# Kernel tuning notes

Measured on AMD Instinct MI355X. Metric: run time of the kernel, lower is better.

The kernel has to match this reference:

```python
import jax, jax.numpy as jnp
import numpy as np
from functools import partial

H = 1024  # lstm_num_hidden
OUT_LEN = 96


def _cell(x, h, c, Wih, Whh, b):
    # PyTorch LSTM cell, gate order (i, f, g, o). x:[B,D] h,c:[B,H]
    g = x @ Wih.T + h @ Whh.T + b
    i, f, gg, o = jnp.split(g, 4, axis=-1)
    i = jax.nn.sigmoid(i)
    f = jax.nn.sigmoid(f)
    o = jax.nn.sigmoid(o)
    c = f * c + i * jnp.tanh(gg)
    h = o * jnp.tanh(c)
    return h, c


def _lstm_layer(xs, Wih, Whh, b):
    # xs: [B, T, D] -> (ys [B,T,H], h_T [B,H], c_T [B,H])
    B = xs.shape[0]
    pre = jnp.einsum('btd,gd->btg', xs, Wih) + b  # precompute input projection

    def step(carry, p):
        h, c = carry
        g = p + h @ Whh.T
        i, f, gg, o = jnp.split(g, 4, axis=-1)
        i = jax.nn.sigmoid(i)
        f = jax.nn.sigmoid(f)
        o = jax.nn.sigmoid(o)
        c = f * c + i * jnp.tanh(gg)
        h = o * jnp.tanh(c)
        return (h, c), h

    h0 = jnp.zeros((B, H), xs.dtype)
    c0 = jnp.zeros((B, H), xs.dtype)
    (h, c), ys = jax.lax.scan(step, (h0, c0), jnp.swapaxes(pre, 0, 1))
    return jnp.swapaxes(ys, 0, 1), h, c


def setup_inputs() -> dict:
    key = jax.random.key(0)
    ks = jax.random.split(key, 16)
    s = 1.0 / np.sqrt(H)  # torch LSTM/Linear init scale
    u = lambda k, shape: jax.random.uniform(k, shape, jnp.float32, -s, s)
    inp = {
        'x': jax.random.normal(ks[0], (256, 336, 1), jnp.float32),
        'enc_Wih0': u(ks[1], (4 * H, 1)),
        'enc_Whh0': u(ks[2], (4 * H, H)),
        'enc_b0': u(ks[3], (4 * H,)),
        'enc_Wih1': u(ks[4], (4 * H, H)),
        'enc_Whh1': u(ks[5], (4 * H, H)),
        'enc_b1': u(ks[6], (4 * H,)),
        'dec_Wih0': u(ks[7], (4 * H, 1)),
        'dec_Whh0': u(ks[8], (4 * H, H)),
        'dec_b0': u(ks[9], (4 * H,)),
        'dec_Wih1': u(ks[10], (4 * H, H)),
        'dec_Whh1': u(ks[11], (4 * H, H)),
        'dec_b1': u(ks[12], (4 * H,)),
        'fc_W': u(ks[13], (1, H)),
        'fc_b': u(ks[14], (1,)),
    }
    return inp


def reference(x, enc_Wih0, enc_Whh0, enc_b0, enc_Wih1, enc_Whh1, enc_b1,
              dec_Wih0, dec_Whh0, dec_b0, dec_Wih1, dec_Whh1, dec_b1,
              fc_W, fc_b):
    # ----- encoder: 2-layer LSTM over x, keep only final (h, c) per layer -----
    ys0, h0, c0 = _lstm_layer(x, enc_Wih0, enc_Whh0, enc_b0)
    _, h1, c1 = _lstm_layer(ys0, enc_Wih1, enc_Whh1, enc_b1)

    xt = x[:, -1, -1:]  # [B, 1] last value of last feature

    def dec_step(carry, _):
        h0, c0, h1, c1, xt = carry
        h0, c0 = _cell(xt, h0, c0, dec_Wih0, dec_Whh0, dec_b0)
        h1, c1 = _cell(h0, h1, c1, dec_Wih1, dec_Whh1, dec_b1)
        y = h1 @ fc_W.T + fc_b  # [B, 1]
        return (h0, c0, h1, c1, y), y

    _, ys = jax.lax.scan(dec_step, (h0, c0, h1, c1, xt), None, length=OUT_LEN)
    return jnp.swapaxes(ys, 0, 1)  # [B, OUT_LEN, 1]
```

## Files before the change

### kernel.cpp

```cpp
#include <hip/hip_runtime.h>

typedef short short8 __attribute__((ext_vector_type(8)));
typedef float f32x4 __attribute__((ext_vector_type(4)));

#define SMEM_BYTES (65536 + 1024)

__device__ __forceinline__ unsigned short f2bf(float x) {
    unsigned int u = __float_as_uint(x);
    u += 0x7FFFu + ((u >> 16) & 1u);
    return (unsigned short)(u >> 16);
}

__device__ __forceinline__ float sigmoidf_(float x) {
    return 1.0f / (1.0f + __expf(-x));
}

__device__ __forceinline__ float tanhf_(float x) {
    float ax = fabsf(x);
    float e = __expf(2.0f * ax);
    float t = 1.0f - 2.0f / (e + 1.0f);
    return copysignf(t, x);
}

__device__ __forceinline__ void gl_lds16(const void* g, void* l) {
    __builtin_amdgcn_global_load_lds(
        (const __attribute__((address_space(1))) void*)g,
        (__attribute__((address_space(3))) void*)l, 16, 0, 0);
}


template<int K>
__device__ __forceinline__ void lstm_tile(
    int idx,
    const unsigned short* __restrict__ A1,
    const unsigned short* __restrict__ A2,
    const unsigned short* __restrict__ W,
    const float* __restrict__ bias,
    const float* __restrict__ xvec, int xstride,
    const float* __restrict__ Wx,
    float* __restrict__ c,
    unsigned short* __restrict__ hout,
    const float* __restrict__ fcW,
    const float* __restrict__ fcb,
    float* __restrict__ yout)
{
    extern __shared__ char smem_raw[];
    float* T0  = (float*)smem_raw;
    float* T1  = (float*)(smem_raw + 17408);
    float* red = (float*)(smem_raw + 65536);

    constexpr int KS = K / 4;
    constexpr int NC = KS / 32;
    constexpr int KC = K / 32;
    const int tid  = threadIdx.x;
    const int lane = tid & 63;
    const int wave = tid >> 6;
    const int g  = idx >> 6;
    const int ug = idx & 63;
    const int mb = g * 64;
    const int ub = ug * 16;

    const unsigned short* Af = (K == 1024) ? A1 : (wave < 2 ? A1 : A2);
    const int kcA0 = (wave * NC) & 31;
    const int kcW0 = wave * NC;
    const unsigned short* ap = Af + ((size_t)(g * 4) * 32 + kcA0) * 512 + lane * 8;
    const unsigned short* bp = W + ((size_t)(ug * KC + kcW0) * 4) * 512 + lane * 8;

    char* stg = smem_raw + wave * 16384;

    f32x4 acc[4][4];
#pragma unroll
    for (int i = 0; i < 4; ++i)
#pragma unroll
        for (int j = 0; j < 4; ++j) acc[i][j] = (f32x4){0.f, 0.f, 0.f, 0.f};

    auto STAGE = [&](int cc, int buf) {
        char* dst = stg + buf * 8192;
        const unsigned short* asrc = ap + cc * 512;
        const unsigned short* bsrc = bp + cc * 2048;
#pragma unroll
        for (int mi = 0; mi < 4; ++mi)
            gl_lds16(asrc + mi * 16384, dst + mi * 1024);
#pragma unroll
        for (int gt = 0; gt < 4; ++gt)
            gl_lds16(bsrc + gt * 512, dst + 4096 + gt * 1024);
    };
    auto CONSUME = [&](int buf) {
        const char* src = stg + buf * 8192;
        short8 a[4], b[4];
#pragma unroll
        for (int p = 0; p < 4; ++p)
            a[p] = *(const short8*)(src + p * 1024 + lane * 16);
#pragma unroll
        for (int p = 0; p < 4; ++p)
            b[p] = *(const short8*)(src + 4096 + p * 1024 + lane * 16);
#pragma unroll
        for (int mi = 0; mi < 4; ++mi)
#pragma unroll
            for (int gt = 0; gt < 4; ++gt)
                acc[mi][gt] = __builtin_amdgcn_mfma_f32_16x16x32_bf16(
                    a[mi], b[gt], acc[mi][gt], 0, 0, 0);
    };

    STAGE(0, 0);
#pragma unroll
    for (int cc = 0; cc < NC; ++cc) {
        STAGE(cc + 1, (cc + 1) & 1);
        asm volatile("s_waitcnt vmcnt(8)" ::: "memory");
        __builtin_amdgcn_sched_barrier(0);
        CONSUME(cc & 1);
    }
    asm volatile("s_waitcnt vmcnt(0)" ::: "memory");
    __syncthreads();

    const int q = lane >> 4;
    const int m = lane & 15;
    float* Tw = (wave & 1) ? T1 : T0;
    if (wave < 2) {
#pragma unroll
        for (int mi = 0; mi < 4; ++mi)
#pragma unroll
            for (int gt = 0; gt < 4; ++gt)
#pragma unroll
                for (int r = 0; r < 4; ++r)
                    Tw[(mi * 16 + q * 4 + r) * 68 + gt * 16 + m] = acc[mi][gt][r];
    }
    __syncthreads();
    if (wave >= 2) {
#pragma unroll
        for (int mi = 0; mi < 4; ++mi)
#pragma unroll
            for (int gt = 0; gt < 4; ++gt)
#pragma unroll
                for (int r = 0; r < 4; ++r)
                    Tw[(mi * 16 + q * 4 + r) * 68 + gt * 16 + m] += acc[mi][gt][r];
    }
    __syncthreads();

    const int lrow = tid >> 2;
    const int uq   = tid & 3;
    const int br   = mb + lrow;
    const int u0   = ub + uq * 4;
    const int toff = lrow * 68 + uq * 4;

    auto gate4 = [&](int gofs) -> float4 {
        float4 a = *(const float4*)(T0 + toff + gofs);
        float4 b = *(const float4*)(T1 + toff + gofs);
        return make_float4(a.x + b.x, a.y + b.y, a.z + b.z, a.w + b.w);
    };
    float4 GI = gate4(0), GF = gate4(16), GG = gate4(32), GO = gate4(48);
    float4 bI = *(const float4*)(bias + u0);
    float4 bF = *(const float4*)(bias + 1024 + u0);
    float4 bG = *(const float4*)(bias + 2048 + u0);
    float4 bO = *(const float4*)(bias + 3072 + u0);
    float4 wI = {0,0,0,0}, wF = {0,0,0,0}, wG = {0,0,0,0}, wO = {0,0,0,0};
    float xv = 0.f;
    if (xvec) {
        xv = xvec[br * xstride];
        wI = *(const float4*)(Wx + u0);
        wF = *(const float4*)(Wx + 1024 + u0);
        wG = *(const float4*)(Wx + 2048 + u0);
        wO = *(const float4*)(Wx + 3072 + u0);
    }
    float4 cc = *(const float4*)(c + (size_t)br * 1024 + u0);

    auto cellc = [&](float gi, float gf, float gg, float go, float cold, float& hO) -> float {
        float i = sigmoidf_(gi);
        float f = sigmoidf_(gf);
        float o = sigmoidf_(go);
        float cn = f * cold + i * tanhf_(gg);
        hO = o * tanhf_(cn);
        return cn;
    };
    float h0v, h1v, h2v, h3v;
    float4 cn;
    cn.x = cellc(GI.x + bI.x + xv * wI.x, GF.x + bF.x + xv * wF.x,
                 GG.x + bG.x + xv * wG.x, GO.x + bO.x + xv * wO.x, cc.x, h0v);
    cn.y = cellc(GI.y + bI.y + xv * wI.y, GF.y + bF.y + xv * wF.y,
                 GG.y + bG.y + xv * wG.y, GO.y + bO.y + xv * wO.y, cc.y, h1v);
    cn.z = cellc(GI.z + bI.z + xv * wI.z, GF.z + bF.z + xv * wF.z,
                 GG.z + bG.z + xv * wG.z, GO.z + bO.z + xv * wO.z, cc.z, h2v);
    cn.w = cellc(GI.w + bI.w + xv * wI.w, GF.w + bF.w + xv * wF.w,
                 GG.w + bG.w + xv * wG.w, GO.w + bO.w + xv * wO.w, cc.w, h3v);
    *(float4*)(c + (size_t)br * 1024 + u0) = cn;

    {
        const int rg = br >> 4, ml = br & 15;
        const int kc = u0 >> 5, qq = (u0 >> 3) & 3, jo = u0 & 7;
        ushort4 hu;
        hu.x = f2bf(h0v); hu.y = f2bf(h1v); hu.z = f2bf(h2v); hu.w = f2bf(h3v);
        *(ushort4*)(hout + ((size_t)(rg * 32 + kc) * 64 + qq * 16 + ml) * 8 + jo) = hu;
    }

    if (fcW) {
        float4 fw = *(const float4*)(fcW + u0);
        float fcp = h0v * fw.x + h1v * fw.y + h2v * fw.z + h3v * fw.w;
        red[uq * 64 + lrow] = fcp;
        __syncthreads();
        if (tid < 64) {
            float s = red[tid] + red[64 + tid] + red[128 + tid] + red[192 + tid];
            if (ub == 0) s += fcb[0];
            atomicAdd(yout + (size_t)(mb + tid) * 96, s);
        }
    }
}

__global__ __launch_bounds__(256)
__attribute__((amdgpu_waves_per_eu(2, 2)))
void k_enc_step(
    int t,
    const float* __restrict__ x,
    const float* __restrict__ Wih0, const float* __restrict__ b0,
    const unsigned short* __restrict__ Wenc0,
    const unsigned short* __restrict__ Wenc1, const float* __restrict__ b1,
    unsigned short* h0a, unsigned short* h0b,
    unsigned short* h1a, unsigned short* h1b,
    float* c0, float* c1)
{
    unsigned short* h0[2] = {h0a, h0b};
    unsigned short* h1[2] = {h1a, h1b};
    const int blk = blockIdx.x;
    if (blk < 256) {
        if (t >= 336) return;
        lstm_tile<1024>(blk, h0[(t + 1) & 1], nullptr, Wenc0, b0,
                        x + t, 336, Wih0, c0, h0[t & 1],
                        nullptr, nullptr, nullptr);
    } else {
        const int u = t - 1;
        if (u < 0) return;
        lstm_tile<2048>(blk - 256, h0[u & 1], h1[(u + 1) & 1], Wenc1, b1,
                        nullptr, 0, nullptr, c1, h1[u & 1],
                        nullptr, nullptr, nullptr);
    }
}

__global__ __launch_bounds__(256)
__attribute__((amdgpu_waves_per_eu(2, 2)))
void k_dec0(
    int s,
    const float* __restrict__ x,
    const float* __restrict__ dout,
    const float* __restrict__ Wih0, const float* __restrict__ b0,
    const unsigned short* __restrict__ Wdec0,
    unsigned short* h0a, unsigned short* h0b, float* c0)
{
    unsigned short* h0[2] = {h0a, h0b};
    const float* xv; int xs;
    if (s == 0) { xv = x + 335; xs = 336; }
    else        { xv = dout + (s - 1); xs = 96; }
    lstm_tile<1024>(blockIdx.x, h0[(s + 1) & 1], nullptr, Wdec0, b0,
                    xv, xs, Wih0, c0, h0[s & 1],
                    nullptr, nullptr, nullptr);
}

__global__ __launch_bounds__(256)
__attribute__((amdgpu_waves_per_eu(2, 2)))
void k_dec1(
    int s,
    const unsigned short* __restrict__ Wdec1, const float* __restrict__ b1,
    unsigned short* h0a, unsigned short* h0b,
    unsigned short* h1a, unsigned short* h1b,
    float* c1,
    const float* __restrict__ fcW, const float* __restrict__ fcb,
    float* __restrict__ dout)
{
    unsigned short* h0[2] = {h0a, h0b};
    unsigned short* h1[2] = {h1a, h1b};
    lstm_tile<2048>(blockIdx.x, h0[s & 1], h1[(s + 1) & 1], Wdec1, b1,
                    nullptr, 0, nullptr, c1, h1[s & 1],
                    fcW, fcb, dout + s);
}

template<int K>
__global__ void k_packW(const float* __restrict__ srcA, const float* __restrict__ srcB,
                        unsigned short* __restrict__ dst)
{
    constexpr int KC = K / 32;
    const int total = 4096 * K / 8;
    const int du = blockIdx.x * blockDim.x + threadIdx.x;
    if (du >= total) return;
    const int lane = du & 63;
    int rest = du >> 6;
    const int gate = rest & 3; rest >>= 2;
    const int kc = rest % KC;
    const int ug = rest / KC;
    const int q = lane >> 4, m = lane & 15;
    const int row = gate * 1024 + ug * 16 + m;
    const int k = kc * 32 + q * 8;
    const float* s;
    if (K == 2048 && k >= 1024) s = srcB + (size_t)row * 1024 + (k - 1024);
    else                        s = srcA + (size_t)row * 1024 + k;
    const float4 v0 = *(const float4*)(s);
    const float4 v1 = *(const float4*)(s + 4);
    short8 o;
    o[0] = (short)f2bf(v0.x); o[1] = (short)f2bf(v0.y);
    o[2] = (short)f2bf(v0.z); o[3] = (short)f2bf(v0.w);
    o[4] = (short)f2bf(v1.x); o[5] = (short)f2bf(v1.y);
    o[6] = (short)f2bf(v1.z); o[7] = (short)f2bf(v1.w);
    *(short8*)(dst + (size_t)du * 8) = o;
}

extern "C" void kernel_launch(void* const* d_in, const int* in_sizes, int n_in,
                              void* d_out, int out_size, void* d_ws, size_t ws_size,
                              hipStream_t stream)
{
    const float* x     = (const float*)d_in[0];
    const float* eWih0 = (const float*)d_in[1];
    const float* eWhh0 = (const float*)d_in[2];
    const float* eb0   = (const float*)d_in[3];
    const float* eWih1 = (const float*)d_in[4];
    const float* eWhh1 = (const float*)d_in[5];
    const float* eb1   = (const float*)d_in[6];
    const float* dWih0 = (const float*)d_in[7];
    const float* dWhh0 = (const float*)d_in[8];
    const float* db0   = (const float*)d_in[9];
    const float* dWih1 = (const float*)d_in[10];
    const float* dWhh1 = (const float*)d_in[11];
    const float* db1   = (const float*)d_in[12];
    const float* fcW   = (const float*)d_in[13];
    const float* fcb   = (const float*)d_in[14];
    float* out = (float*)d_out;

    char* ws = (char*)d_ws;
    size_t off = 0;
    auto walloc = [&](size_t bytes) -> void* {
        void* p = ws + off;
        off = (off + bytes + 255) & ~(size_t)255;
        return p;
    };
    unsigned short* Wenc0 = (unsigned short*)walloc((size_t)4096 * 1024 * 2 + 32768);
    unsigned short* Wenc1 = (unsigned short*)walloc((size_t)4096 * 2048 * 2 + 32768);
    unsigned short* Wdec0 = (unsigned short*)walloc((size_t)4096 * 1024 * 2 + 32768);
    unsigned short* Wdec1 = (unsigned short*)walloc((size_t)4096 * 2048 * 2 + 32768);
    const size_t STATE = (size_t)4 * 524288 + (size_t)2 * 1048576;
    char* stateBase = (char*)walloc(STATE + 65536);
    unsigned short* h0a = (unsigned short*)(stateBase);
    unsigned short* h0b = (unsigned short*)(stateBase + 524288);
    unsigned short* h1a = (unsigned short*)(stateBase + 2 * 524288);
    unsigned short* h1b = (unsigned short*)(stateBase + 3 * 524288);
    float* c0 = (float*)(stateBase + 4 * 524288);
    float* c1 = (float*)(stateBase + 4 * 524288 + 1048576);

    hipMemsetAsync(stateBase, 0, STATE, stream);
    hipMemsetAsync(d_out, 0, (size_t)out_size * sizeof(float), stream);

    {
        const int n1 = 4096 * 1024 / 8;
        const int n2 = 4096 * 2048 / 8;
        k_packW<1024><<<n1 / 256, 256, 0, stream>>>(eWhh0, nullptr, Wenc0);
        k_packW<1024><<<n1 / 256, 256, 0, stream>>>(dWhh0, nullptr, Wdec0);
        k_packW<2048><<<n2 / 256, 256, 0, stream>>>(eWih1, eWhh1, Wenc1);
        k_packW<2048><<<n2 / 256, 256, 0, stream>>>(dWih1, dWhh1, Wdec1);
    }

    for (int t = 0; t <= 336; ++t) {
        k_enc_step<<<512, 256, SMEM_BYTES, stream>>>(t, x, eWih0, eb0, Wenc0, Wenc1, eb1,
                                                     h0a, h0b, h1a, h1b, c0, c1);
    }
    for (int s = 0; s < 96; ++s) {
        k_dec0<<<256, 256, SMEM_BYTES, stream>>>(s, x, out, dWih0, db0, Wdec0, h0a, h0b, c0);
        k_dec1<<<256, 256, SMEM_BYTES, stream>>>(s, Wdec1, db1, h0a, h0b, h1a, h1b, c1,
                                                 fcW, fcb, out);
    }
}
```

Baseline: 6.660 ms.

## Widen encoder tiles to 128 batch rows per block sharing weight loads

The encoder step kernel now runs 512-thread blocks, each covering 128 batch rows (two 64-row halves) for the same 16-unit weight slice. This halves the number of blocks and halves how often each weight tile is re-fetched across the batch. In exchange, each block needs 128 KB of LDS for the widened staging and partial-sum buffers, which limits occupancy to one block per CU and gives fewer, larger blocks. Decoder kernels keep the original 64-row tiling.

```diff
diff --git a/kernel.cpp b/kernel.cpp
--- a/kernel.cpp
+++ b/kernel.cpp
@@ -3,7 +3,8 @@
 typedef short short8 __attribute__((ext_vector_type(8)));
 typedef float f32x4 __attribute__((ext_vector_type(4)));
 
-#define SMEM_BYTES (65536 + 1024)
+#define SMEM_NARROW (65536 + 1024)
+#define SMEM_WIDE   (131072)
 
 __device__ __forceinline__ unsigned short f2bf(float x) {
     unsigned int u = __float_as_uint(x);
@@ -29,7 +30,7 @@
 }
 
 
-template<int K>
+template<int K, int MH>
 __device__ __forceinline__ void lstm_tile(
     int idx,
     const unsigned short* __restrict__ A1,
@@ -45,25 +46,27 @@
     float* __restrict__ yout)
 {
     extern __shared__ char smem_raw[];
-    float* T0  = (float*)smem_raw;
-    float* T1  = (float*)(smem_raw + 17408);
-    float* red = (float*)(smem_raw + 65536);
-
+    float* Tbase = (float*)smem_raw;
+
+    constexpr int ROWS = 64 * MH;
     constexpr int KS = K / 4;
     constexpr int NC = KS / 32;
     constexpr int KC = K / 32;
     const int tid  = threadIdx.x;
     const int lane = tid & 63;
     const int wave = tid >> 6;
+    const int kq   = wave & 3;
+    const int mh   = wave >> 2;
     const int g  = idx >> 6;
     const int ug = idx & 63;
-    const int mb = g * 64;
+    const int mb = g * ROWS;
     const int ub = ug * 16;
 
-    const unsigned short* Af = (K == 1024) ? A1 : (wave < 2 ? A1 : A2);
-    const int kcA0 = (wave * NC) & 31;
-    const int kcW0 = wave * NC;
-    const unsigned short* ap = Af + ((size_t)(g * 4) * 32 + kcA0) * 512 + lane * 8;
+    const unsigned short* Af = (K == 1024) ? A1 : (kq < 2 ? A1 : A2);
+    const int kcA0 = (kq * NC) & 31;
+    const int kcW0 = kq * NC;
+    const int rgbase = (g * MH + mh) * 4;
+    const unsigned short* ap = Af + ((size_t)(rgbase * 32 + kcA0)) * 512 + lane * 8;
     const unsigned short* bp = W + ((size_t)(ug * KC + kcW0) * 4) * 512 + lane * 8;
 
     char* stg = smem_raw + wave * 16384;
@@ -115,8 +118,8 @@
 
     const int q = lane >> 4;
     const int m = lane & 15;
-    float* Tw = (wave & 1) ? T1 : T0;
-    if (wave < 2) {
+    float* Tw = Tbase + (mh * 2 + (kq & 1)) * (64 * 68);
+    if (kq < 2) {
 #pragma unroll
         for (int mi = 0; mi < 4; ++mi)
 #pragma unroll
@@ -126,7 +129,7 @@
                     Tw[(mi * 16 + q * 4 + r) * 68 + gt * 16 + m] = acc[mi][gt][r];
     }
     __syncthreads();
-    if (wave >= 2) {
+    if (kq >= 2) {
 #pragma unroll
         for (int mi = 0; mi < 4; ++mi)
 #pragma unroll
@@ -139,13 +142,17 @@
 
     const int lrow = tid >> 2;
     const int uq   = tid & 3;
+    const int th   = lrow >> 6;
+    const int lr   = lrow & 63;
     const int br   = mb + lrow;
     const int u0   = ub + uq * 4;
-    const int toff = lrow * 68 + uq * 4;
+    const int toff = lr * 68 + uq * 4;
+    const float* Ta = Tbase + (th * 2) * (64 * 68);
+    const float* Tb = Tbase + (th * 2 + 1) * (64 * 68);
 
     auto gate4 = [&](int gofs) -> float4 {
-        float4 a = *(const float4*)(T0 + toff + gofs);
-        float4 b = *(const float4*)(T1 + toff + gofs);
+        float4 a = *(const float4*)(Ta + toff + gofs);
+        float4 b = *(const float4*)(Tb + toff + gofs);
         return make_float4(a.x + b.x, a.y + b.y, a.z + b.z, a.w + b.w);
     };
     float4 GI = gate4(0), GF = gate4(16), GG = gate4(32), GO = gate4(48);
@@ -193,6 +200,7 @@
     }
 
     if (fcW) {
+        float* red = (float*)(smem_raw + 65536);
         float4 fw = *(const float4*)(fcW + u0);
         float fcp = h0v * fw.x + h1v * fw.y + h2v * fw.z + h3v * fw.w;
         red[uq * 64 + lrow] = fcp;
@@ -205,7 +213,7 @@
     }
 }
 
-__global__ __launch_bounds__(256)
+__global__ __launch_bounds__(512)
 __attribute__((amdgpu_waves_per_eu(2, 2)))
 void k_enc_step(
     int t,
@@ -220,17 +228,17 @@
     unsigned short* h0[2] = {h0a, h0b};
     unsigned short* h1[2] = {h1a, h1b};
     const int blk = blockIdx.x;
-    if (blk < 256) {
+    if (blk < 128) {
         if (t >= 336) return;
-        lstm_tile<1024>(blk, h0[(t + 1) & 1], nullptr, Wenc0, b0,
-                        x + t, 336, Wih0, c0, h0[t & 1],
-                        nullptr, nullptr, nullptr);
+        lstm_tile<1024, 2>(blk, h0[(t + 1) & 1], nullptr, Wenc0, b0,
+                           x + t, 336, Wih0, c0, h0[t & 1],
+                           nullptr, nullptr, nullptr);
     } else {
         const int u = t - 1;
         if (u < 0) return;
-        lstm_tile<2048>(blk - 256, h0[u & 1], h1[(u + 1) & 1], Wenc1, b1,
-                        nullptr, 0, nullptr, c1, h1[u & 1],
-                        nullptr, nullptr, nullptr);
+        lstm_tile<2048, 2>(blk - 128, h0[u & 1], h1[(u + 1) & 1], Wenc1, b1,
+                           nullptr, 0, nullptr, c1, h1[u & 1],
+                           nullptr, nullptr, nullptr);
     }
 }
 
@@ -248,9 +256,9 @@
     const float* xv; int xs;
     if (s == 0) { xv = x + 335; xs = 336; }
     else        { xv = dout + (s - 1); xs = 96; }
-    lstm_tile<1024>(blockIdx.x, h0[(s + 1) & 1], nullptr, Wdec0, b0,
-                    xv, xs, Wih0, c0, h0[s & 1],
-                    nullptr, nullptr, nullptr);
+    lstm_tile<1024, 1>(blockIdx.x, h0[(s + 1) & 1], nullptr, Wdec0, b0,
+                       xv, xs, Wih0, c0, h0[s & 1],
+                       nullptr, nullptr, nullptr);
 }
 
 __global__ __launch_bounds__(256)
@@ -266,9 +274,9 @@
 {
     unsigned short* h0[2] = {h0a, h0b};
     unsigned short* h1[2] = {h1a, h1b};
-    lstm_tile<2048>(blockIdx.x, h0[s & 1], h1[(s + 1) & 1], Wdec1, b1,
-                    nullptr, 0, nullptr, c1, h1[s & 1],
-                    fcW, fcb, dout + s);
+    lstm_tile<2048, 1>(blockIdx.x, h0[s & 1], h1[(s + 1) & 1], Wdec1, b1,
+                       nullptr, 0, nullptr, c1, h1[s & 1],
+                       fcW, fcb, dout + s);
 }
 
 template<int K>
@@ -354,12 +362,12 @@
     }
 
     for (int t = 0; t <= 336; ++t) {
-        k_enc_step<<<512, 256, SMEM_BYTES, stream>>>(t, x, eWih0, eb0, Wenc0, Wenc1, eb1,
-                                                     h0a, h0b, h1a, h1b, c0, c1);
+        k_enc_step<<<256, 512, SMEM_WIDE, stream>>>(t, x, eWih0, eb0, Wenc0, Wenc1, eb1,
+                                                    h0a, h0b, h1a, h1b, c0, c1);
     }
     for (int s = 0; s < 96; ++s) {
-        k_dec0<<<256, 256, SMEM_BYTES, stream>>>(s, x, out, dWih0, db0, Wdec0, h0a, h0b, c0);
-        k_dec1<<<256, 256, SMEM_BYTES, stream>>>(s, Wdec1, db1, h0a, h0b, h1a, h1b, c1,
-                                                 fcW, fcb, out);
-    }
-}
+        k_dec0<<<256, 256, SMEM_NARROW, stream>>>(s, x, out, dWih0, db0, Wdec0, h0a, h0b, c0);
+        k_dec1<<<256, 256, SMEM_NARROW, stream>>>(s, Wdec1, db1, h0a, h0b, h1a, h1b, c1,
+                                                  fcW, fcb, out);
+    }
+}
```

Result: slower. 7.229 ms (+8.5%).
